# Optimization experiments

Hardware: AMD Instinct MI355X
Metric: run time of the kernel (lower is better)

The kernel has to match this reference:

```python
import jax, jax.numpy as jnp
import numpy as np

OUTPUT_SIZE = (7, 7)
SPATIAL_SCALE = 0.25
SAMPLING_RATIO = 2


def setup_inputs() -> dict:
    key = jax.random.key(0)
    k1, k2, k3, k4, k5 = jax.random.split(key, 5)
    N, C, H, W = 2, 256, 200, 304
    R = 1000
    features = jax.random.normal(k1, (N, C, H, W), dtype=jnp.float32)
    # Boxes in IMAGE coordinates (image ~ 800x1216 since spatial_scale=0.25)
    img_h, img_w = H / SPATIAL_SCALE, W / SPATIAL_SCALE
    batch_idx = jax.random.randint(k2, (R,), 0, N).astype(jnp.float32)
    x1 = jax.random.uniform(k3, (R,), minval=0.0, maxval=img_w * 0.8)
    y1 = jax.random.uniform(k4, (R,), minval=0.0, maxval=img_h * 0.8)
    wh = jax.random.uniform(k5, (R, 2), minval=16.0, maxval=256.0)
    x2 = jnp.minimum(x1 + wh[:, 0], img_w - 1.0)
    y2 = jnp.minimum(y1 + wh[:, 1], img_h - 1.0)
    boxes = jnp.stack([batch_idx, x1, y1, x2, y2], axis=1).astype(jnp.float32)
    return {"features": features, "boxes": boxes}


def _axis_interp(coord, size):
    """torchvision bilinear_interpolate clamping along one axis.
    coord: float sample positions. Returns (low_idx, high_idx, frac, valid)."""
    valid = (coord >= -1.0) & (coord <= size)
    c = jnp.maximum(coord, 0.0)
    low_raw = jnp.floor(c).astype(jnp.int32)
    at_edge = low_raw >= size - 1
    low = jnp.where(at_edge, size - 1, low_raw)
    high = jnp.where(at_edge, size - 1, low_raw + 1)
    frac = jnp.where(at_edge, 0.0, c - low_raw.astype(c.dtype))
    return low, high, frac, valid


def roi_align(features, boxes, output_size, spatial_scale, sampling_ratio):
    N, C, H, W = features.shape
    PH, PW = output_size
    G = sampling_ratio
    b = boxes[:, 0].astype(jnp.int32)                      # [R]
    x1 = boxes[:, 1] * spatial_scale
    y1 = boxes[:, 2] * spatial_scale
    x2 = boxes[:, 3] * spatial_scale
    y2 = boxes[:, 4] * spatial_scale
    roi_w = jnp.maximum(x2 - x1, 1.0)
    roi_h = jnp.maximum(y2 - y1, 1.0)
    bin_h = roi_h / PH
    bin_w = roi_w / PW
    off = (jnp.arange(G, dtype=jnp.float32) + 0.5) / G     # [G] sample offsets in bin
    # per-axis sample coords: ys [R,PH,G], xs [R,PW,G]
    ys = y1[:, None, None] + (jnp.arange(PH, dtype=jnp.float32)[None, :, None] + off[None, None, :]) * bin_h[:, None, None]
    xs = x1[:, None, None] + (jnp.arange(PW, dtype=jnp.float32)[None, :, None] + off[None, None, :]) * bin_w[:, None, None]
    yl, yh, fy, vy = _axis_interp(ys, H)
    xl, xh, fx, vx = _axis_interp(xs, W)
    feat = features.transpose(0, 2, 3, 1)                  # [N,H,W,C]
    bb = b[:, None, None, None, None]                      # broadcast to [R,PH,G,PW,G]
    Y = lambda idx: idx[:, :, :, None, None]
    X = lambda idx: idx[:, None, None, :, :]
    # four corner gathers -> [R,PH,G,PW,G,C]
    v_ll = feat[bb, Y(yl), X(xl)]
    v_lh = feat[bb, Y(yl), X(xh)]
    v_hl = feat[bb, Y(yh), X(xl)]
    v_hh = feat[bb, Y(yh), X(xh)]
    fy_b = fy[:, :, :, None, None, None]
    fx_b = fx[:, None, None, :, :, None]
    interp = ((1 - fy_b) * (1 - fx_b) * v_ll + (1 - fy_b) * fx_b * v_lh
              + fy_b * (1 - fx_b) * v_hl + fy_b * fx_b * v_hh)
    valid = (vy[:, :, :, None, None] & vx[:, None, None, :, :])[..., None]
    interp = jnp.where(valid, interp, 0.0)
    pooled = interp.mean(axis=(2, 4))                      # avg over G*G samples -> [R,PH,PW,C]
    return pooled.transpose(0, 3, 1, 2)                    # [R,C,PH,PW]


def reference(features, boxes):
    return roi_align(features, boxes, OUTPUT_SIZE, SPATIAL_SCALE, SAMPLING_RATIO)
```

## Files before the change

kernel.cpp:

```cpp
#include <hip/hip_runtime.h>
#include <hip/hip_bf16.h>


constexpr int N_B  = 2;
constexpr int C_CH = 256;
constexpr int H_F  = 200;
constexpr int W_F  = 304;
constexpr int HW   = H_F * W_F;
constexpr int PH   = 7;
constexpr int PW   = 7;
constexpr int CELLS = PH * PW;
constexpr float SCALE = 0.25f;

static __device__ __forceinline__ unsigned short f2bf(float f) {
    __hip_bfloat16 h = __float2bfloat16(f);
    return *reinterpret_cast<unsigned short*>(&h);
}
static __device__ __forceinline__ float bf2f(unsigned short u) {
    return __uint_as_float(((unsigned int)u) << 16);
}

__global__ __launch_bounds__(256) void transpose_nchw_nhwc_bf16(
    const float* __restrict__ in, unsigned short* __restrict__ out)
{
    __shared__ float tile[64][65];
    int tx = blockIdx.x * 64;
    int ty = blockIdx.y * 64;
    int n  = blockIdx.z;
    const float* ip = in  + (size_t)n * C_CH * HW;
    unsigned short* op = out + (size_t)n * HW * C_CH;

    int w4 = threadIdx.x & 15;
    int cr = threadIdx.x >> 4;
#pragma unroll
    for (int p = 0; p < 4; ++p) {
        int c = p * 16 + cr;
        float4 v = *(const float4*)&ip[(size_t)(ty + c) * HW + tx + 4 * w4];
        tile[c][4 * w4 + 0] = v.x;
        tile[c][4 * w4 + 1] = v.y;
        tile[c][4 * w4 + 2] = v.z;
        tile[c][4 * w4 + 3] = v.w;
    }
    __syncthreads();
    int cq = threadIdx.x & 15;
    int hr = threadIdx.x >> 4;
#pragma unroll
    for (int p = 0; p < 4; ++p) {
        int hw = p * 16 + hr;
        ushort4 v;
        v.x = f2bf(tile[4 * cq + 0][hw]);
        v.y = f2bf(tile[4 * cq + 1][hw]);
        v.z = f2bf(tile[4 * cq + 2][hw]);
        v.w = f2bf(tile[4 * cq + 3][hw]);
        *(ushort4*)&op[(size_t)(tx + hw) * C_CH + ty + 4 * cq] = v;
    }
}

__global__ __launch_bounds__(512) void roi_gather_nhwc(
    const unsigned short* __restrict__ feat_nhwc,
    const float* __restrict__ boxes,
    float* __restrict__ out, int R)
{
    __shared__ alignas(16) float lds[C_CH * CELLS];
    int r = blockIdx.x;
    if (r >= R) return;
    int tid  = threadIdx.x;
    int wave = tid >> 6;
    int lane = tid & 63;

    const float* box = boxes + r * 5;
    int   b  = (int)box[0];
    float x1 = box[1] * SCALE;
    float y1 = box[2] * SCALE;
    float x2 = box[3] * SCALE;
    float y2 = box[4] * SCALE;
    float bin_w = fmaxf(x2 - x1, 1.0f) * (1.0f / PW);
    float bin_h = fmaxf(y2 - y1, 1.0f) * (1.0f / PH);

    const unsigned short* fb = feat_nhwc + (size_t)b * HW * C_CH + 4 * lane;

    for (int cell = wave; cell < CELLS; cell += 8) {
        int ph = cell / PW;
        int pw = cell - ph * PW;

        int   yl[2], yh[2]; float fy[2], vy[2];
#pragma unroll
        for (int iy = 0; iy < 2; ++iy) {
            float y = y1 + ((float)ph + (iy ? 0.75f : 0.25f)) * bin_h;
            vy[iy] = (y >= -1.0f && y <= (float)H_F) ? 1.0f : 0.0f;
            float cy = fmaxf(y, 0.0f);
            int ylr = (int)floorf(cy);
            bool e = (ylr >= H_F - 1);
            yl[iy] = e ? H_F - 1 : ylr;
            yh[iy] = e ? H_F - 1 : ylr + 1;
            fy[iy] = e ? 0.0f : cy - (float)ylr;
        }
        int   xl[2], xh[2]; float fx[2], vx[2];
#pragma unroll
        for (int ix = 0; ix < 2; ++ix) {
            float x = x1 + ((float)pw + (ix ? 0.75f : 0.25f)) * bin_w;
            vx[ix] = (x >= -1.0f && x <= (float)W_F) ? 1.0f : 0.0f;
            float cx = fmaxf(x, 0.0f);
            int xlr = (int)floorf(cx);
            bool e = (xlr >= W_F - 1);
            xl[ix] = e ? W_F - 1 : xlr;
            xh[ix] = e ? W_F - 1 : xlr + 1;
            fx[ix] = e ? 0.0f : cx - (float)xlr;
        }

        ushort4 t[16];
#pragma unroll
        for (int iy = 0; iy < 2; ++iy) {
#pragma unroll
            for (int ix = 0; ix < 2; ++ix) {
                int i = (iy * 2 + ix) * 4;
                t[i + 0] = *(const ushort4*)(fb + (size_t)(yl[iy] * W_F + xl[ix]) * C_CH);
                t[i + 1] = *(const ushort4*)(fb + (size_t)(yl[iy] * W_F + xh[ix]) * C_CH);
                t[i + 2] = *(const ushort4*)(fb + (size_t)(yh[iy] * W_F + xl[ix]) * C_CH);
                t[i + 3] = *(const ushort4*)(fb + (size_t)(yh[iy] * W_F + xh[ix]) * C_CH);
            }
        }

        float a0 = 0.0f, a1 = 0.0f, a2 = 0.0f, a3 = 0.0f;
#pragma unroll
        for (int iy = 0; iy < 2; ++iy) {
#pragma unroll
            for (int ix = 0; ix < 2; ++ix) {
                int i = (iy * 2 + ix) * 4;
                float w   = vy[iy] * vx[ix];
                float fxx = fx[ix];
                float fyy = fy[iy];
                float lo, hi;
                lo = bf2f(t[i+0].x) + fxx * (bf2f(t[i+1].x) - bf2f(t[i+0].x));
                hi = bf2f(t[i+2].x) + fxx * (bf2f(t[i+3].x) - bf2f(t[i+2].x));
                a0 += w * (lo + fyy * (hi - lo));
                lo = bf2f(t[i+0].y) + fxx * (bf2f(t[i+1].y) - bf2f(t[i+0].y));
                hi = bf2f(t[i+2].y) + fxx * (bf2f(t[i+3].y) - bf2f(t[i+2].y));
                a1 += w * (lo + fyy * (hi - lo));
                lo = bf2f(t[i+0].z) + fxx * (bf2f(t[i+1].z) - bf2f(t[i+0].z));
                hi = bf2f(t[i+2].z) + fxx * (bf2f(t[i+3].z) - bf2f(t[i+2].z));
                a2 += w * (lo + fyy * (hi - lo));
                lo = bf2f(t[i+0].w) + fxx * (bf2f(t[i+1].w) - bf2f(t[i+0].w));
                hi = bf2f(t[i+2].w) + fxx * (bf2f(t[i+3].w) - bf2f(t[i+2].w));
                a3 += w * (lo + fyy * (hi - lo));
            }
        }

        int cbase = 4 * lane;
        lds[(cbase + 0) * CELLS + cell] = a0 * 0.25f;
        lds[(cbase + 1) * CELLS + cell] = a1 * 0.25f;
        lds[(cbase + 2) * CELLS + cell] = a2 * 0.25f;
        lds[(cbase + 3) * CELLS + cell] = a3 * 0.25f;
    }
    __syncthreads();

    const float4* src = (const float4*)lds;
    float4* dst = (float4*)(out + (size_t)r * (C_CH * CELLS));
#pragma unroll
    for (int i = tid; i < (C_CH * CELLS) / 4; i += 512) {
        dst[i] = src[i];
    }
}

__global__ __launch_bounds__(256) void roi_align_fallback(
    const float* __restrict__ feat,
    const float* __restrict__ boxes,
    float* __restrict__ out, int total)
{
    int idx = blockIdx.x * 256 + threadIdx.x;
    if (idx >= total) return;
    int pw = idx % PW;
    int t  = idx / PW;
    int ph = t % PH;
    t /= PH;
    int c = t & (C_CH - 1);
    int r = t >> 8;

    const float* box = boxes + r * 5;
    int   b  = (int)box[0];
    float x1 = box[1] * SCALE;
    float y1 = box[2] * SCALE;
    float x2 = box[3] * SCALE;
    float y2 = box[4] * SCALE;
    float bin_w = fmaxf(x2 - x1, 1.0f) * (1.0f / PW);
    float bin_h = fmaxf(y2 - y1, 1.0f) * (1.0f / PH);
    const float* fp = feat + ((size_t)b * C_CH + c) * HW;

    float acc = 0.0f;
#pragma unroll
    for (int iy = 0; iy < 2; ++iy) {
        float y = y1 + ((float)ph + (iy ? 0.75f : 0.25f)) * bin_h;
        bool vy = (y >= -1.0f) && (y <= (float)H_F);
        float cy = fmaxf(y, 0.0f);
        int ylr = (int)floorf(cy);
        int yl, yh; float fy;
        if (ylr >= H_F - 1) { yl = H_F - 1; yh = H_F - 1; fy = 0.0f; }
        else                { yl = ylr;     yh = ylr + 1; fy = cy - (float)ylr; }
#pragma unroll
        for (int ix = 0; ix < 2; ++ix) {
            float x = x1 + ((float)pw + (ix ? 0.75f : 0.25f)) * bin_w;
            bool vx = (x >= -1.0f) && (x <= (float)W_F);
            float cx = fmaxf(x, 0.0f);
            int xlr = (int)floorf(cx);
            int xl, xh; float fx;
            if (xlr >= W_F - 1) { xl = W_F - 1; xh = W_F - 1; fx = 0.0f; }
            else                { xl = xlr;     xh = xlr + 1; fx = cx - (float)xlr; }
            if (vy && vx) {
                const float* rl = fp + yl * W_F;
                const float* rh = fp + yh * W_F;
                float vll = rl[xl], vlh = rl[xh], vhl = rh[xl], vhh = rh[xh];
                float vlo = vll + fx * (vlh - vll);
                float vhi = vhl + fx * (vhh - vhl);
                acc += vlo + fy * (vhi - vlo);
            }
        }
    }
    out[idx] = acc * 0.25f;
}

extern "C" void kernel_launch(void* const* d_in, const int* in_sizes, int n_in,
                              void* d_out, int out_size, void* d_ws, size_t ws_size,
                              hipStream_t stream) {
    const float* feat  = (const float*)d_in[0];
    const float* boxes = (const float*)d_in[1];
    float* out = (float*)d_out;
    int R = in_sizes[1] / 5;

    size_t need = (size_t)N_B * C_CH * HW * sizeof(unsigned short);
    if (ws_size >= need) {
        unsigned short* nhwc = (unsigned short*)d_ws;
        dim3 tg(HW / 64, C_CH / 64, N_B);
        transpose_nchw_nhwc_bf16<<<tg, 256, 0, stream>>>(feat, nhwc);
        roi_gather_nhwc<<<R, 512, 0, stream>>>(nhwc, boxes, out, R);
    } else {
        int total = out_size;
        roi_align_fallback<<<(total + 255) / 256, 256, 0, stream>>>(feat, boxes, out, total);
    }
}
```

Baseline: 242.9 us.

## Widen ROI gather loads to 16B per lane and swizzle padded LDS staging

The gather kernel now uses 32-lane groups, each lane loading 8 bf16 channels as a uint4. Each wave therefore processes two cells at once with fewer, wider load instructions, and the bf16 unpacking works on packed 32-bit words. The LDS staging buffer is padded to a stride of 56 and the cell index is XOR-swizzled to cut bank conflicts on the transposed writes, at the cost of a per-element divide and index math on the readback. Nontemporal loads in the transpose and nontemporal stores on the output are added to reduce cache pollution.

New measurement: 233.3 us. 4.0% less time.

```diff
diff --git a/kernel.cpp b/kernel.cpp
--- a/kernel.cpp
+++ b/kernel.cpp
@@ -10,14 +10,21 @@
 constexpr int PH   = 7;
 constexpr int PW   = 7;
 constexpr int CELLS = PH * PW;
+constexpr int CSTRIDE = 56;
 constexpr float SCALE = 0.25f;
+
+typedef float  v4f __attribute__((ext_vector_type(4)));
+typedef unsigned int v4u __attribute__((ext_vector_type(4)));
 
 static __device__ __forceinline__ unsigned short f2bf(float f) {
     __hip_bfloat16 h = __float2bfloat16(f);
     return *reinterpret_cast<unsigned short*>(&h);
 }
-static __device__ __forceinline__ float bf2f(unsigned short u) {
-    return __uint_as_float(((unsigned int)u) << 16);
+static __device__ __forceinline__ float blo(unsigned int u) {
+    return __uint_as_float(u << 16);
+}
+static __device__ __forceinline__ float bhi(unsigned int u) {
+    return __uint_as_float(u & 0xffff0000u);
 }
 
 __global__ __launch_bounds__(256) void transpose_nchw_nhwc_bf16(
@@ -35,7 +42,8 @@
 #pragma unroll
     for (int p = 0; p < 4; ++p) {
         int c = p * 16 + cr;
-        float4 v = *(const float4*)&ip[(size_t)(ty + c) * HW + tx + 4 * w4];
+        v4f v = __builtin_nontemporal_load(
+            (const v4f*)&ip[(size_t)(ty + c) * HW + tx + 4 * w4]);
         tile[c][4 * w4 + 0] = v.x;
         tile[c][4 * w4 + 1] = v.y;
         tile[c][4 * w4 + 2] = v.z;
@@ -56,17 +64,36 @@
     }
 }
 
+static __device__ __forceinline__ void acc8(
+    float* acc, uint4 ll, uint4 lh, uint4 hl, uint4 hh,
+    float fxx, float fyy, float w)
+{
+#define ACC_PAIR(C, I0, I1)                                                   \
+    { float a = blo(ll.C), b = blo(lh.C), c = blo(hl.C), d = blo(hh.C);       \
+      float lo = a + fxx * (b - a), hi = c + fxx * (d - c);                   \
+      acc[I0] += w * (lo + fyy * (hi - lo)); }                                \
+    { float a = bhi(ll.C), b = bhi(lh.C), c = bhi(hl.C), d = bhi(hh.C);       \
+      float lo = a + fxx * (b - a), hi = c + fxx * (d - c);                   \
+      acc[I1] += w * (lo + fyy * (hi - lo)); }
+    ACC_PAIR(x, 0, 1)
+    ACC_PAIR(y, 2, 3)
+    ACC_PAIR(z, 4, 5)
+    ACC_PAIR(w, 6, 7)
+#undef ACC_PAIR
+}
+
 __global__ __launch_bounds__(512) void roi_gather_nhwc(
     const unsigned short* __restrict__ feat_nhwc,
     const float* __restrict__ boxes,
     float* __restrict__ out, int R)
 {
-    __shared__ alignas(16) float lds[C_CH * CELLS];
+    __shared__ alignas(16) float lds[C_CH * CSTRIDE];
     int r = blockIdx.x;
     if (r >= R) return;
-    int tid  = threadIdx.x;
-    int wave = tid >> 6;
-    int lane = tid & 63;
+    int tid = threadIdx.x;
+    int grp = tid >> 5;
+    int ln  = tid & 31;
+    int swz = ln & 7;
 
     const float* box = boxes + r * 5;
     int   b  = (int)box[0];
@@ -77,9 +104,9 @@
     float bin_w = fmaxf(x2 - x1, 1.0f) * (1.0f / PW);
     float bin_h = fmaxf(y2 - y1, 1.0f) * (1.0f / PH);
 
-    const unsigned short* fb = feat_nhwc + (size_t)b * HW * C_CH + 4 * lane;
-
-    for (int cell = wave; cell < CELLS; cell += 8) {
+    const unsigned short* fb = feat_nhwc + (size_t)b * HW * C_CH + 8 * ln;
+
+    for (int cell = grp; cell < CELLS; cell += 16) {
         int ph = cell / PW;
         int pw = cell - ph * PW;
 
@@ -108,57 +135,52 @@
             fx[ix] = e ? 0.0f : cx - (float)xlr;
         }
 
-        ushort4 t[16];
+        float acc[8] = {0.f, 0.f, 0.f, 0.f, 0.f, 0.f, 0.f, 0.f};
+
 #pragma unroll
         for (int iy = 0; iy < 2; ++iy) {
-#pragma unroll
-            for (int ix = 0; ix < 2; ++ix) {
-                int i = (iy * 2 + ix) * 4;
-                t[i + 0] = *(const ushort4*)(fb + (size_t)(yl[iy] * W_F + xl[ix]) * C_CH);
-                t[i + 1] = *(const ushort4*)(fb + (size_t)(yl[iy] * W_F + xh[ix]) * C_CH);
-                t[i + 2] = *(const ushort4*)(fb + (size_t)(yh[iy] * W_F + xl[ix]) * C_CH);
-                t[i + 3] = *(const ushort4*)(fb + (size_t)(yh[iy] * W_F + xh[ix]) * C_CH);
-            }
-        }
-
-        float a0 = 0.0f, a1 = 0.0f, a2 = 0.0f, a3 = 0.0f;
-#pragma unroll
-        for (int iy = 0; iy < 2; ++iy) {
-#pragma unroll
-            for (int ix = 0; ix < 2; ++ix) {
-                int i = (iy * 2 + ix) * 4;
-                float w   = vy[iy] * vx[ix];
-                float fxx = fx[ix];
-                float fyy = fy[iy];
-                float lo, hi;
-                lo = bf2f(t[i+0].x) + fxx * (bf2f(t[i+1].x) - bf2f(t[i+0].x));
-                hi = bf2f(t[i+2].x) + fxx * (bf2f(t[i+3].x) - bf2f(t[i+2].x));
-                a0 += w * (lo + fyy * (hi - lo));
-                lo = bf2f(t[i+0].y) + fxx * (bf2f(t[i+1].y) - bf2f(t[i+0].y));
-                hi = bf2f(t[i+2].y) + fxx * (bf2f(t[i+3].y) - bf2f(t[i+2].y));
-                a1 += w * (lo + fyy * (hi - lo));
-                lo = bf2f(t[i+0].z) + fxx * (bf2f(t[i+1].z) - bf2f(t[i+0].z));
-                hi = bf2f(t[i+2].z) + fxx * (bf2f(t[i+3].z) - bf2f(t[i+2].z));
-                a2 += w * (lo + fyy * (hi - lo));
-                lo = bf2f(t[i+0].w) + fxx * (bf2f(t[i+1].w) - bf2f(t[i+0].w));
-                hi = bf2f(t[i+2].w) + fxx * (bf2f(t[i+3].w) - bf2f(t[i+2].w));
-                a3 += w * (lo + fyy * (hi - lo));
-            }
-        }
-
-        int cbase = 4 * lane;
-        lds[(cbase + 0) * CELLS + cell] = a0 * 0.25f;
-        lds[(cbase + 1) * CELLS + cell] = a1 * 0.25f;
-        lds[(cbase + 2) * CELLS + cell] = a2 * 0.25f;
-        lds[(cbase + 3) * CELLS + cell] = a3 * 0.25f;
+            const unsigned short* rl = fb + (size_t)(yl[iy] * W_F) * C_CH;
+            const unsigned short* rh = fb + (size_t)(yh[iy] * W_F) * C_CH;
+            uint4 l0 = *(const uint4*)(rl + (size_t)xl[0] * C_CH);
+            uint4 l1 = *(const uint4*)(rl + (size_t)xh[0] * C_CH);
+            uint4 l2 = *(const uint4*)(rl + (size_t)xl[1] * C_CH);
+            uint4 l3 = *(const uint4*)(rl + (size_t)xh[1] * C_CH);
+            uint4 h0 = *(const uint4*)(rh + (size_t)xl[0] * C_CH);
+            uint4 h1 = *(const uint4*)(rh + (size_t)xh[0] * C_CH);
+            uint4 h2 = *(const uint4*)(rh + (size_t)xl[1] * C_CH);
+            uint4 h3 = *(const uint4*)(rh + (size_t)xh[1] * C_CH);
+            acc8(acc, l0, l1, h0, h1, fx[0], fy[iy], vy[iy] * vx[0]);
+            acc8(acc, l2, l3, h2, h3, fx[1], fy[iy], vy[iy] * vx[1]);
+        }
+
+        int cellx = cell ^ swz;
+#pragma unroll
+        for (int j = 0; j < 8; ++j)
+            lds[(8 * ln + j) * CSTRIDE + cellx] = acc[j] * 0.25f;
     }
     __syncthreads();
 
-    const float4* src = (const float4*)lds;
-    float4* dst = (float4*)(out + (size_t)r * (C_CH * CELLS));
-#pragma unroll
-    for (int i = tid; i < (C_CH * CELLS) / 4; i += 512) {
-        dst[i] = src[i];
+    v4f* dst = (v4f*)(out + (size_t)r * (C_CH * CELLS));
+    for (int q = tid; q < (C_CH * CELLS) / 4; q += 512) {
+        int w0 = 4 * q;
+        v4f v;
+        {
+            int c = w0 / 49, ce = w0 - 49 * c;
+            v.x = lds[c * CSTRIDE + (ce ^ ((c >> 3) & 7))];
+        }
+        {
+            int wv = w0 + 1; int c = wv / 49, ce = wv - 49 * c;
+            v.y = lds[c * CSTRIDE + (ce ^ ((c >> 3) & 7))];
+        }
+        {
+            int wv = w0 + 2; int c = wv / 49, ce = wv - 49 * c;
+            v.z = lds[c * CSTRIDE + (ce ^ ((c >> 3) & 7))];
+        }
+        {
+            int wv = w0 + 3; int c = wv / 49, ce = wv - 49 * c;
+            v.w = lds[c * CSTRIDE + (ce ^ ((c >> 3) & 7))];
+        }
+        __builtin_nontemporal_store(v, dst + q);
     }
 }
 
@@ -193,25 +215,25 @@
         bool vy = (y >= -1.0f) && (y <= (float)H_F);
         float cy = fmaxf(y, 0.0f);
         int ylr = (int)floorf(cy);
-        int yl, yh; float fy;
-        if (ylr >= H_F - 1) { yl = H_F - 1; yh = H_F - 1; fy = 0.0f; }
-        else                { yl = ylr;     yh = ylr + 1; fy = cy - (float)ylr; }
+        int yl, yh; float fyv;
+        if (ylr >= H_F - 1) { yl = H_F - 1; yh = H_F - 1; fyv = 0.0f; }
+        else                { yl = ylr;     yh = ylr + 1; fyv = cy - (float)ylr; }
 #pragma unroll
         for (int ix = 0; ix < 2; ++ix) {
             float x = x1 + ((float)pw + (ix ? 0.75f : 0.25f)) * bin_w;
             bool vx = (x >= -1.0f) && (x <= (float)W_F);
             float cx = fmaxf(x, 0.0f);
             int xlr = (int)floorf(cx);
-            int xl, xh; float fx;
-            if (xlr >= W_F - 1) { xl = W_F - 1; xh = W_F - 1; fx = 0.0f; }
-            else                { xl = xlr;     xh = xlr + 1; fx = cx - (float)xlr; }
+            int xlv, xhv; float fxv;
+            if (xlr >= W_F - 1) { xlv = W_F - 1; xhv = W_F - 1; fxv = 0.0f; }
+            else                { xlv = xlr;     xhv = xlr + 1; fxv = cx - (float)xlr; }
             if (vy && vx) {
                 const float* rl = fp + yl * W_F;
                 const float* rh = fp + yh * W_F;
-                float vll = rl[xl], vlh = rl[xh], vhl = rh[xl], vhh = rh[xh];
-                float vlo = vll + fx * (vlh - vll);
-                float vhi = vhl + fx * (vhh - vhl);
-                acc += vlo + fy * (vhi - vlo);
+                float vll = rl[xlv], vlh = rl[xhv], vhl = rh[xlv], vhh = rh[xhv];
+                float vlo = vll + fxv * (vlh - vll);
+                float vhi = vhl + fxv * (vhh - vhl);
+                acc += vlo + fyv * (vhi - vlo);
             }
         }
     }
```
